# Kernel tuning notes

Measured on AMD Instinct MI355X. Metric: run time of the kernel, lower is better.

Reference implementation:

```python
import jax, jax.numpy as jnp
import numpy as np

B, C, P, HP, WP = 128, 3, 196, 16, 16  # batch, channels, patches, patch h, patch w
E = 768  # embedding size; patches_pixel_count = C*HP*WP = 768


def setup_inputs() -> dict:
    key = jax.random.key(0)
    ks = jax.random.split(key, 9)
    return {
        "inputs": jax.random.normal(ks[0], (B, C, P, HP, WP), dtype=jnp.float32),
        "W1": jax.random.normal(ks[1], (C * HP * WP, 32), dtype=jnp.float32) * 0.02,
        "b1": jax.random.normal(ks[2], (32,), dtype=jnp.float32) * 0.02,
        "W2": jax.random.normal(ks[3], (32, 64), dtype=jnp.float32) * 0.02,
        "b2": jax.random.normal(ks[4], (64,), dtype=jnp.float32) * 0.02,
        "W3": jax.random.normal(ks[5], (64, E), dtype=jnp.float32) * 0.02,
        "b3": jax.random.normal(ks[6], (E,), dtype=jnp.float32) * 0.02,
        "cls_token": jax.random.normal(ks[7], (1, E), dtype=jnp.float32) * 0.02,
        "pos_enc": jax.random.normal(ks[8], (P + 1, E), dtype=jnp.float32) * 0.02,
    }


def reference(inputs, W1, b1, W2, b2, W3, b3, cls_token, pos_enc):
    b, c, p, hp, wp = inputs.shape
    # per-patch slab is [C, hp, wp] flattened in (C, h, w) order -> [B, P, C*hp*wp]
    x = jnp.transpose(inputs, (0, 2, 1, 3, 4)).reshape(b, p, c * hp * wp)
    x = x @ W1 + b1          # [B, P, 32]
    x = x @ W2 + b2          # [B, P, 64]
    x = x @ W3 + b3          # [B, P, E]
    cls = jnp.broadcast_to(cls_token[None], (b, 1, cls_token.shape[-1]))
    x = jnp.concatenate([cls, x], axis=1)  # [B, P+1, E]
    return x + pos_enc[None]               # broadcast add of position encodings
```

## Files before the change

### kernel.cpp

```cpp
#include <hip/hip_runtime.h>


#define BATCH 128
#define CH    3
#define NP    196
#define PIX   256
#define K1    768
#define NH    64
#define EMB   768
#define NROW  (BATCH * NP)

typedef __bf16 bf16x8 __attribute__((ext_vector_type(8)));
typedef __bf16 bf16x4 __attribute__((ext_vector_type(4)));
typedef float  f32x4  __attribute__((ext_vector_type(4)));

#define W12T_OFF 0
#define W3T_OFF  98304
#define BF_OFF   196608
#define H_OFF    199680

__global__ __launch_bounds__(256) void patchembed_prep(
    const float* __restrict__ W1, const float* __restrict__ W2,
    const float* __restrict__ b1, const float* __restrict__ b2,
    const float* __restrict__ W3, const float* __restrict__ b3,
    const float* __restrict__ cls, const float* __restrict__ pos,
    __bf16* __restrict__ w12t, __bf16* __restrict__ w3t,
    float* __restrict__ bf, float* __restrict__ out)
{
    const int i = blockIdx.x * 256 + threadIdx.x;
    const int T0 = NH * K1;
    const int T1 = T0 + EMB;
    const int T2 = T1 + EMB * NH;

    if (i < T0) {
        const int n = i / K1, k = i - n * K1;
        float s = 0.f;
        #pragma unroll
        for (int j = 0; j < 32; ++j) s += W1[k * 32 + j] * W2[j * NH + n];
        w12t[i] = (__bf16)s;
    } else if (i < T1) {
        const int c = i - T0;
        float s = b3[c];
        for (int n = 0; n < NH; ++n) {
            float t = b2[n];
            #pragma unroll
            for (int j = 0; j < 32; ++j) t += b1[j] * W2[j * NH + n];
            s += t * W3[n * EMB + c];
        }
        bf[c] = s;
    } else if (i < T2) {
        const int j = i - T1;
        const int col = j >> 6, kk = j & 63;
        w3t[j] = (__bf16)W3[kk * EMB + col];
    } else {
        const int j = i - T2;
        const int b = j / EMB, c = j - b * EMB;
        out[b * (197 * EMB) + c] = cls[c] + pos[c];
    }
}

__global__ __launch_bounds__(256) void patchembed_s1(
    const float* __restrict__ X,
    const __bf16* __restrict__ w12t,
    __bf16* __restrict__ H)
{
    __shared__ __align__(16) float h1p[4][16][68];

    const int tid  = threadIdx.x;
    const int wv   = tid >> 6;
    const int lane = tid & 63;
    const int l15  = lane & 15;
    const int q    = lane >> 4;
    const int r0   = blockIdx.x * 16;

    {
        const int xrow = r0 + l15;
        const int b = xrow / NP, p = xrow - b * NP;
        const float* xb = X + ((b * CH) * NP + p) * PIX;
        const int kb0 = wv * 6;

        f32x4 acc0 = {0.f, 0.f, 0.f, 0.f};
        f32x4 acc1 = acc0, acc2 = acc0, acc3 = acc0;
        #pragma unroll
        for (int t = 0; t < 6; ++t) {
            const int kb = kb0 + t;
            const float* ptr = xb + (kb >> 3) * (NP * PIX) + (kb & 7) * 32 + q * 8;
            float4 u = *(const float4*)ptr;
            float4 v = *(const float4*)(ptr + 4);
            bf16x8 a;
            a[0] = (__bf16)u.x; a[1] = (__bf16)u.y;
            a[2] = (__bf16)u.z; a[3] = (__bf16)u.w;
            a[4] = (__bf16)v.x; a[5] = (__bf16)v.y;
            a[6] = (__bf16)v.z; a[7] = (__bf16)v.w;
            const __bf16* wb = w12t + kb * 32 + q * 8;
            bf16x8 f0 = *(const bf16x8*)(wb + l15 * K1);
            bf16x8 f1 = *(const bf16x8*)(wb + (16 + l15) * K1);
            bf16x8 f2 = *(const bf16x8*)(wb + (32 + l15) * K1);
            bf16x8 f3 = *(const bf16x8*)(wb + (48 + l15) * K1);
            acc0 = __builtin_amdgcn_mfma_f32_16x16x32_bf16(a, f0, acc0, 0, 0, 0);
            acc1 = __builtin_amdgcn_mfma_f32_16x16x32_bf16(a, f1, acc1, 0, 0, 0);
            acc2 = __builtin_amdgcn_mfma_f32_16x16x32_bf16(a, f2, acc2, 0, 0, 0);
            acc3 = __builtin_amdgcn_mfma_f32_16x16x32_bf16(a, f3, acc3, 0, 0, 0);
        }
        #pragma unroll
        for (int r = 0; r < 4; ++r) {
            h1p[wv][q * 4 + r][l15]      = acc0[r];
            h1p[wv][q * 4 + r][16 + l15] = acc1[r];
            h1p[wv][q * 4 + r][32 + l15] = acc2[r];
            h1p[wv][q * 4 + r][48 + l15] = acc3[r];
        }
    }
    __syncthreads();

    {
        const int c0 = wv * 16 + q * 4;
        f32x4 s = {0.f, 0.f, 0.f, 0.f};
        #pragma unroll
        for (int w = 0; w < 4; ++w)
            s += *(const f32x4*)&h1p[w][l15][c0];
        bf16x4 hv;
        #pragma unroll
        for (int j = 0; j < 4; ++j) hv[j] = (__bf16)s[j];
        *(bf16x4*)(H + (r0 + l15) * NH + c0) = hv;
    }
}

__global__ __launch_bounds__(256) void patchembed_s2(
    const __bf16* __restrict__ H,
    const __bf16* __restrict__ w3t,
    const float*  __restrict__ bf,
    const float*  __restrict__ pos,
    float* __restrict__ out)
{
    const int tid  = threadIdx.x;
    const int wv   = tid >> 6;
    const int lane = tid & 63;
    const int l15  = lane & 15;
    const int q    = lane >> 4;

    const int wave_id = blockIdx.x * 4 + wv;
    const int rt = wave_id >> 3;
    const int cs = wave_id & 7;
    const int r0 = rt * 16;

    const __bf16* hr = H + (r0 + l15) * NH;
    bf16x8 hb0 = *(const bf16x8*)(hr + q * 8);
    bf16x8 hb1 = *(const bf16x8*)(hr + 32 + q * 8);

    const int row = r0 + l15;
    const int b = row / NP, p = row - b * NP;
    float* orow = out + (b * 197 + p + 1) * EMB;
    const float* prow = pos + (p + 1) * EMB;

    #pragma unroll
    for (int t = 0; t < 6; ++t) {
        const int colb = cs * 96 + t * 16;
        const __bf16* wr = w3t + (colb + l15) * NH;
        bf16x8 wa0 = *(const bf16x8*)(wr + q * 8);
        bf16x8 wa1 = *(const bf16x8*)(wr + 32 + q * 8);
        f32x4 z = {0.f, 0.f, 0.f, 0.f};
        f32x4 c = __builtin_amdgcn_mfma_f32_16x16x32_bf16(wa0, hb0, z, 0, 0, 0);
        c       = __builtin_amdgcn_mfma_f32_16x16x32_bf16(wa1, hb1, c, 0, 0, 0);
        const int c4 = colb + q * 4;
        f32x4 pv = *(const f32x4*)(prow + c4);
        f32x4 bv = *(const f32x4*)(bf + c4);
        *(f32x4*)(orow + c4) = c + pv + bv;
    }
}

extern "C" void kernel_launch(void* const* d_in, const int* in_sizes, int n_in,
                              void* d_out, int out_size, void* d_ws, size_t ws_size,
                              hipStream_t stream)
{
    const float* X   = (const float*)d_in[0];
    const float* W1  = (const float*)d_in[1];
    const float* b1  = (const float*)d_in[2];
    const float* W2  = (const float*)d_in[3];
    const float* b2  = (const float*)d_in[4];
    const float* W3  = (const float*)d_in[5];
    const float* b3  = (const float*)d_in[6];
    const float* cls = (const float*)d_in[7];
    const float* pos = (const float*)d_in[8];
    float* out = (float*)d_out;

    char* ws = (char*)d_ws;
    __bf16* w12t = (__bf16*)(ws + W12T_OFF);
    __bf16* w3t  = (__bf16*)(ws + W3T_OFF);
    float*  bf   = (float*)(ws + BF_OFF);
    __bf16* H    = (__bf16*)(ws + H_OFF);

    patchembed_prep<<<771, 256, 0, stream>>>(W1, W2, b1, b2, W3, b3, cls, pos,
                                             w12t, w3t, bf, out);
    patchembed_s1<<<NROW / 16, 256, 0, stream>>>(X, w12t, H);
    patchembed_s2<<<NROW / 16 * 2, 256, 0, stream>>>(H, w3t, bf, pos, out);
}
```

Measured before the change: 212.3 us.

## Stage patch tiles into LDS via direct global loads and drop split-K reduction

The first-stage kernel now copies each block's 16 patch rows (768 fp32 values each) straight into shared memory with global_load_lds. Each wave then computes 16 of the 64 hidden outputs over the full K dimension. This replaces the earlier scheme, where each wave did a K-slice for all 64 outputs and a shared-memory cross-wave reduction followed. The goal is better coalesced, asynchronous loads of the large input and no reduction pass. In exchange it uses about 49KB of LDS per block, adds a launch-bounds occupancy hint of three blocks, and its strided LDS reads may cause bank conflicts.

```diff
diff --git a/kernel.cpp b/kernel.cpp
--- a/kernel.cpp
+++ b/kernel.cpp
@@ -18,6 +18,11 @@
 #define W3T_OFF  98304
 #define BF_OFF   196608
 #define H_OFF    199680
+
+#define GLOAD_LDS16(g, l)                                                  \
+    __builtin_amdgcn_global_load_lds(                                      \
+        (const __attribute__((address_space(1))) unsigned int*)(g),        \
+        (__attribute__((address_space(3))) unsigned int*)(l), 16, 0, 0)
 
 __global__ __launch_bounds__(256) void patchembed_prep(
     const float* __restrict__ W1, const float* __restrict__ W2,
@@ -59,12 +64,12 @@
     }
 }
 
-__global__ __launch_bounds__(256) void patchembed_s1(
+__global__ __launch_bounds__(256, 3) void patchembed_s1(
     const float* __restrict__ X,
     const __bf16* __restrict__ w12t,
     __bf16* __restrict__ H)
 {
-    __shared__ __align__(16) float h1p[4][16][68];
+    __shared__ __align__(16) float xs[16][772];
 
     const int tid  = threadIdx.x;
     const int wv   = tid >> 6;
@@ -73,56 +78,41 @@
     const int q    = lane >> 4;
     const int r0   = blockIdx.x * 16;
 
-    {
-        const int xrow = r0 + l15;
-        const int b = xrow / NP, p = xrow - b * NP;
-        const float* xb = X + ((b * CH) * NP + p) * PIX;
-        const int kb0 = wv * 6;
+    const int b0 = r0 / NP;
+    const int p0 = r0 - b0 * NP;
 
-        f32x4 acc0 = {0.f, 0.f, 0.f, 0.f};
-        f32x4 acc1 = acc0, acc2 = acc0, acc3 = acc0;
-        #pragma unroll
-        for (int t = 0; t < 6; ++t) {
-            const int kb = kb0 + t;
-            const float* ptr = xb + (kb >> 3) * (NP * PIX) + (kb & 7) * 32 + q * 8;
-            float4 u = *(const float4*)ptr;
-            float4 v = *(const float4*)(ptr + 4);
-            bf16x8 a;
-            a[0] = (__bf16)u.x; a[1] = (__bf16)u.y;
-            a[2] = (__bf16)u.z; a[3] = (__bf16)u.w;
-            a[4] = (__bf16)v.x; a[5] = (__bf16)v.y;
-            a[6] = (__bf16)v.z; a[7] = (__bf16)v.w;
-            const __bf16* wb = w12t + kb * 32 + q * 8;
-            bf16x8 f0 = *(const bf16x8*)(wb + l15 * K1);
-            bf16x8 f1 = *(const bf16x8*)(wb + (16 + l15) * K1);
-            bf16x8 f2 = *(const bf16x8*)(wb + (32 + l15) * K1);
-            bf16x8 f3 = *(const bf16x8*)(wb + (48 + l15) * K1);
-            acc0 = __builtin_amdgcn_mfma_f32_16x16x32_bf16(a, f0, acc0, 0, 0, 0);
-            acc1 = __builtin_amdgcn_mfma_f32_16x16x32_bf16(a, f1, acc1, 0, 0, 0);
-            acc2 = __builtin_amdgcn_mfma_f32_16x16x32_bf16(a, f2, acc2, 0, 0, 0);
-            acc3 = __builtin_amdgcn_mfma_f32_16x16x32_bf16(a, f3, acc3, 0, 0, 0);
-        }
-        #pragma unroll
-        for (int r = 0; r < 4; ++r) {
-            h1p[wv][q * 4 + r][l15]      = acc0[r];
-            h1p[wv][q * 4 + r][16 + l15] = acc1[r];
-            h1p[wv][q * 4 + r][32 + l15] = acc2[r];
-            h1p[wv][q * 4 + r][48 + l15] = acc3[r];
-        }
+    #pragma unroll
+    for (int i = 0; i < 12; ++i) {
+        const int chunk = wv * 12 + i;
+        const int c   = chunk >> 4;
+        const int row = chunk & 15;
+        int p = p0 + row, b = b0;
+        if (p >= NP) { p -= NP; b += 1; }
+        const float* gp = X + (((b * CH) + c) * NP + p) * PIX + lane * 4;
+        GLOAD_LDS16(gp, &xs[row][c * 256]);
     }
     __syncthreads();
 
-    {
-        const int c0 = wv * 16 + q * 4;
-        f32x4 s = {0.f, 0.f, 0.f, 0.f};
-        #pragma unroll
-        for (int w = 0; w < 4; ++w)
-            s += *(const f32x4*)&h1p[w][l15][c0];
-        bf16x4 hv;
-        #pragma unroll
-        for (int j = 0; j < 4; ++j) hv[j] = (__bf16)s[j];
-        *(bf16x4*)(H + (r0 + l15) * NH + c0) = hv;
+    const __bf16* wrow = w12t + (wv * 16 + l15) * K1;
+    const float*  xrow = &xs[l15][0];
+    f32x4 acc = {0.f, 0.f, 0.f, 0.f};
+    #pragma unroll
+    for (int ks = 0; ks < 24; ++ks) {
+        bf16x8 a = *(const bf16x8*)(wrow + ks * 32 + q * 8);
+        const float* xp = xrow + ks * 32 + q * 8;
+        f32x4 u = *(const f32x4*)xp;
+        f32x4 v = *(const f32x4*)(xp + 4);
+        bf16x8 xb;
+        xb[0] = (__bf16)u[0]; xb[1] = (__bf16)u[1];
+        xb[2] = (__bf16)u[2]; xb[3] = (__bf16)u[3];
+        xb[4] = (__bf16)v[0]; xb[5] = (__bf16)v[1];
+        xb[6] = (__bf16)v[2]; xb[7] = (__bf16)v[3];
+        acc = __builtin_amdgcn_mfma_f32_16x16x32_bf16(a, xb, acc, 0, 0, 0);
     }
+    bf16x4 hv;
+    #pragma unroll
+    for (int j = 0; j < 4; ++j) hv[j] = (__bf16)acc[j];
+    *(bf16x4*)(H + (r0 + l15) * NH + wv * 16 + q * 4) = hv;
 }
 
 __global__ __launch_bounds__(256) void patchembed_s2(
```

Measured after the change: 208.9 us. No clear change (-1.6%).
